# Optimization experiments

Measured on AMD Instinct MI355X. Metric: run time of the kernel, lower is better.

The kernel has to match this reference:

```python
import jax, jax.numpy as jnp
import numpy as np


def _adder2d(x, w, stride, padding):
    """AdderNet 'convolution': out[b,o,i,j] = -sum_p |patch[b,p,i,j] - w[o,p]|.

    x: [B, C, H, W], w: [O, C, kh, kw]. Patches are extracted in (C, kh, kw)
    channel-major order, matching torch.nn.functional.unfold / w.reshape(O, -1).
    """
    O, C, kh, kw = w.shape
    patches = jax.lax.conv_general_dilated_patches(
        x, (kh, kw), (stride, stride), [(padding, padding), (padding, padding)])
    B, P, Ho, Wo = patches.shape  # P = C*kh*kw
    p = patches.reshape(B, P, Ho * Wo)
    wf = w.reshape(O, P)

    def per_out(wo):  # sequential over small O to avoid a [B,O,P,L] blowup
        return -jnp.sum(jnp.abs(p - wo[None, :, None]), axis=1)  # [B, L]

    out = jax.lax.map(per_out, wf)  # [O, B, L]
    return jnp.transpose(out, (1, 0, 2)).reshape(B, O, Ho, Wo)


def setup_inputs() -> dict:
    key = jax.random.key(0)
    ks = jax.random.split(key, 5)
    x = jax.random.normal(ks[0], (4096, 1, 28, 28), dtype=jnp.float32)
    w1 = jax.random.normal(ks[1], (16, 1, 3, 3), dtype=jnp.float32)
    w2 = jax.random.normal(ks[2], (32, 16, 3, 3), dtype=jnp.float32)
    w3 = jax.random.normal(ks[3], (16, 32, 3, 3), dtype=jnp.float32)
    w4 = jax.random.normal(ks[4], (10, 16, 3, 3), dtype=jnp.float32)
    return {"x": x, "w1": w1, "w2": w2, "w3": w3, "w4": w4}


def reference(x, w1, w2, w3, w4):
    h = x - 0.5
    h = jax.nn.relu((_adder2d(h, w1, 2, 0) + 10.0) / 4.0)   # [B,16,13,13]
    h = jax.nn.relu((_adder2d(h, w2, 2, 1) + 130.0) / 8.0)  # [B,32,7,7]
    h = jax.nn.relu((_adder2d(h, w3, 2, 1) + 280.0) / 16.0)  # [B,16,4,4]
    h = _adder2d(h, w4, 2, 0)                                # [B,10,1,1]
    h = h.reshape(h.shape[0], -1)                            # [B,10]
    return jax.nn.log_softmax(h, axis=1)
```

## Files before the change

kernel.cpp:

```cpp
#include <hip/hip_runtime.h>
#include <math.h>


#if defined(__has_builtin)
#if __has_builtin(__builtin_amdgcn_sad_u16)
#define HAS_SAD 1
#endif
#endif

__device__ __forceinline__ unsigned sadu16(unsigned a, unsigned b, unsigned acc) {
#ifdef HAS_SAD
  return __builtin_amdgcn_sad_u16(a, b, acc);
#else
  int al = (int)(a & 0xFFFFu), ah = (int)(a >> 16);
  int bl = (int)(b & 0xFFFFu), bh = (int)(b >> 16);
  return acc + (unsigned)(al > bl ? al - bl : bl - al)
             + (unsigned)(ah > bh ? ah - bh : bh - ah);
#endif
}

__device__ __forceinline__ unsigned quant(float v) {
  return (unsigned)fmaf(v, 1024.0f, 8192.5f);
}
__device__ __forceinline__ unsigned quantx(float v) {
  return (unsigned)fmaf(v, 1024.0f, 7680.5f);
}
__device__ __forceinline__ int imax(int a, int b) { return a > b ? a : b; }
__device__ __forceinline__ int yoff1(int y) { return y * 19 + (y >> 1); }
__device__ __forceinline__ int yoff2(int y) { return y * 9 + (y >> 1); }

#define QPAD 0x20002000u

__global__ void adder_prep(const float* __restrict__ w1, const float* __restrict__ w2,
                           const float* __restrict__ w3, const float* __restrict__ w4,
                           unsigned* __restrict__ qw) {
  int k = blockIdx.x * 256 + threadIdx.x;
  if (k < 96) {
    int o = k / 6, r = k % 6, kh = r >> 1, h = r & 1;
    const float* p = w1 + o * 9 + kh * 3;
    qw[k] = h ? quant(p[2]) : (quant(p[0]) | (quant(p[1]) << 16));
  } else if (k < 2400) {
    int k2 = k - 96, m = k2 / 288, r = k2 % 288, o = r / 9, pk = r % 9;
    int s = o * 144 + 2 * m * 9 + pk;
    qw[k] = quant(w2[s]) | (quant(w2[s + 9]) << 16);
  } else if (k < 4704) {
    int k3 = k - 2400, m2 = k3 / 144, r = k3 % 144, o = r / 9, pk = r % 9;
    int s = o * 288 + 2 * m2 * 9 + pk;
    qw[k] = quant(w3[s]) | (quant(w3[s + 9]) << 16);
  } else if (k < 5424) {
    int k4 = k - 4704, m = k4 / 90, r = k4 % 90, o = r / 9, pk = r % 9;
    int s = o * 144 + 2 * m * 9 + pk;
    qw[k] = quant(w4[s]) | (quant(w4[s + 9]) << 16);
  }
}

__global__ __launch_bounds__(128, 6) void adder_main(
    const float* __restrict__ gx,
    const unsigned* __restrict__ qw,
    float* __restrict__ gout)
{
  __shared__ __align__(16) unsigned sA1[2304];
  __shared__ __align__(16) unsigned sA2[1360];

  const int t = threadIdx.x;
  const int l = t & 63;
  const int wu = __builtin_amdgcn_readfirstlane(t >> 6);
  const int b = blockIdx.x;
  const float* img = gx + (size_t)b * 784;

  for (int k = t; k < 448; k += 128) {
    int plane = k / 56, c = k % 56;
    int y, x;
    if (c < 15)      { y = 0;      x = c; }
    else if (c < 30) { y = 14;     x = c - 15; }
    else if (c < 43) { y = c - 29; x = 0; }
    else             { y = c - 42; x = 14; }
    sA1[plane * 288 + yoff1(y) + x] = QPAD;
  }

  if (l < 52) {
    const int i = l >> 2, jq = l & 3;
    unsigned r[3][5], mw[3][4];
#pragma unroll
    for (int kh = 0; kh < 3; ++kh) {
      const float* rp = img + (2 * i + kh) * 28 + 8 * jq;
      float4 A = *(const float4*)(rp);
      float4 B = *(const float4*)(rp + 4);
      float2 C = *(const float2*)(rp + 8);
      r[kh][0] = quantx(A.x) | (quantx(A.y) << 16);
      r[kh][1] = quantx(A.z) | (quantx(A.w) << 16);
      r[kh][2] = quantx(B.x) | (quantx(B.y) << 16);
      r[kh][3] = quantx(B.z) | (quantx(B.w) << 16);
      r[kh][4] = quantx(C.x) | (quantx(C.y) << 16);
#pragma unroll
      for (int c = 0; c < 4; ++c) mw[kh][c] = r[kh][c + 1] & 0xFFFFu;
    }
    const int dbase = yoff1(i + 1) + 4 * jq + 1;
#pragma unroll 2
    for (int opp = 0; opp < 4; ++opp) {
      const int op = wu * 4 + opp;
      const unsigned* w = qw + op * 12;
      unsigned a0[4], a1[4];
#pragma unroll
      for (int jj = 0; jj < 4; ++jj) { a0[jj] = 0u; a1[jj] = 0u; }
#pragma unroll
      for (int kh = 0; kh < 3; ++kh) {
        unsigned wa01 = w[kh * 2], wa2 = w[kh * 2 + 1];
        unsigned wb01 = w[6 + kh * 2], wb2 = w[6 + kh * 2 + 1];
#pragma unroll
        for (int jj = 0; jj < 4; ++jj) {
          a0[jj] = sadu16(r[kh][jj], wa01, a0[jj]);
          a0[jj] = sadu16(mw[kh][jj], wa2, a0[jj]);
          a1[jj] = sadu16(r[kh][jj], wb01, a1[jj]);
          a1[jj] = sadu16(mw[kh][jj], wb2, a1[jj]);
        }
      }
      unsigned* dst = sA1 + op * 288 + dbase;
#pragma unroll
      for (int jj = 0; jj < 4; ++jj) {
        if (4 * jq + jj < 13) {
          int q0 = imax(10752 - (int)((a0[jj] + 2u) >> 2), 8192);
          int q1 = imax(10752 - (int)((a1[jj] + 2u) >> 2), 8192);
          dst[jj] = (unsigned)q0 | ((unsigned)q1 << 16);
        }
      }
    }
  }
  __syncthreads();

  for (int k = t; k < 512; k += 128) {
    int plane = k >> 5, c = k & 31;
    int y, x;
    if (c < 9)       { y = 0; x = c; }
    else if (c < 18) { y = 8; x = c - 9; }
    else if (c < 25) { y = c - 17; x = 0; }
    else             { y = c - 24; x = 8; }
    sA2[plane * 85 + yoff2(y) + x] = QPAD;
  }

  if (l < 49) {
    const int i = l / 7, j = l % 7;
    unsigned acc[16];
#pragma unroll
    for (int o = 0; o < 16; ++o) acc[o] = 0u;
    const unsigned* qw2 = qw + 96 + wu * 144;
    const unsigned* pb = sA1 + 39 * i + 2 * j;
    const int K1o[3] = {0, 19, 39};
    unsigned p[3][3];
#pragma unroll
    for (int kh = 0; kh < 3; ++kh)
#pragma unroll
      for (int c = 0; c < 3; ++c)
        p[kh][c] = pb[K1o[kh] + c];
#pragma unroll 1
    for (int m = 0; m < 8; ++m) {
      unsigned pn[3][3];
      const unsigned* pbn = pb + (((m + 1) & 7) * 288);
#pragma unroll
      for (int kh = 0; kh < 3; ++kh)
#pragma unroll
        for (int c = 0; c < 3; ++c)
          pn[kh][c] = pbn[K1o[kh] + c];
      const unsigned* wm = qw2 + m * 288;
#pragma unroll
      for (int o = 0; o < 16; ++o) {
        const unsigned* w9 = wm + o * 9;
        unsigned a = acc[o];
#pragma unroll
        for (int kh = 0; kh < 3; ++kh)
#pragma unroll
          for (int c = 0; c < 3; ++c)
            a = sadu16(p[kh][c], w9[kh * 3 + c], a);
        acc[o] = a;
      }
#pragma unroll
      for (int kh = 0; kh < 3; ++kh)
#pragma unroll
        for (int c = 0; c < 3; ++c)
          p[kh][c] = pn[kh][c];
    }
#pragma unroll
    for (int m2 = 0; m2 < 8; ++m2) {
      int q0 = imax(24832 - (int)((acc[2 * m2] + 4u) >> 3), 8192);
      int q1 = imax(24832 - (int)((acc[2 * m2 + 1] + 4u) >> 3), 8192);
      sA2[(wu * 8 + m2) * 85 + yoff2(i + 1) + (j + 1)] = (unsigned)q0 | ((unsigned)q1 << 16);
    }
  }
  __syncthreads();

  {
    const int pos = l & 15, oq = l >> 4;
    const int i = pos >> 2, j = pos & 3;
    const int pr = wu * 4 + oq;
    const unsigned* qw3 = qw + 2400 + pr * 18;
    unsigned acc0 = 0u, acc1 = 0u;
    const unsigned* pb = sA2 + 19 * i + 2 * j;
    const int K2o[3] = {0, 9, 19};
    unsigned p[3][3];
#pragma unroll
    for (int kh = 0; kh < 3; ++kh)
#pragma unroll
      for (int c = 0; c < 3; ++c)
        p[kh][c] = pb[K2o[kh] + c];
#pragma unroll 1
    for (int m2 = 0; m2 < 16; ++m2) {
      unsigned pn[3][3];
      const unsigned* pbn = pb + (((m2 + 1) & 15) * 85);
#pragma unroll
      for (int kh = 0; kh < 3; ++kh)
#pragma unroll
        for (int c = 0; c < 3; ++c)
          pn[kh][c] = pbn[K2o[kh] + c];
      const unsigned* w18 = qw3 + m2 * 144;
#pragma unroll
      for (int kh = 0; kh < 3; ++kh)
#pragma unroll
        for (int c = 0; c < 3; ++c) {
          acc0 = sadu16(p[kh][c], w18[kh * 3 + c], acc0);
          acc1 = sadu16(p[kh][c], w18[9 + kh * 3 + c], acc1);
        }
#pragma unroll
      for (int kh = 0; kh < 3; ++kh)
#pragma unroll
        for (int c = 0; c < 3; ++c)
          p[kh][c] = pn[kh][c];
    }
    int q0 = imax(26112 - (int)((acc0 + 8u) >> 4), 8192);
    int q1 = imax(26112 - (int)((acc1 + 8u) >> 4), 8192);
    sA1[pr * 17 + pos] = (unsigned)q0 | ((unsigned)q1 << 16);
  }
  __syncthreads();

  if (t < 40) {
    const int o = t % 10, mq = t / 10;
    const unsigned* qw4 = qw + 4704;
    unsigned acc = 0u;
#pragma unroll
    for (int mm = 0; mm < 2; ++mm) {
      const int m = mq * 2 + mm;
      const unsigned* a3 = sA1 + m * 17;
      const unsigned* w9 = qw4 + (m * 10 + o) * 9;
#pragma unroll
      for (int kh = 0; kh < 3; ++kh)
#pragma unroll
        for (int kw = 0; kw < 3; ++kw)
          acc = sadu16(a3[kh * 4 + kw], w9[kh * 3 + kw], acc);
    }
    sA1[200 + t] = acc;
  }
  __syncthreads();
  if (t < 10) {
    unsigned s = sA1[200 + t] + sA1[210 + t] + sA1[220 + t] + sA1[230 + t];
    ((float*)sA1)[248 + t] = -(float)s * (1.0f / 1024.0f);
  }
  __syncthreads();
  if (t < 10) {
    const float* lg = (const float*)sA1 + 248;
    float mx = lg[0];
#pragma unroll
    for (int k = 1; k < 10; ++k) mx = fmaxf(mx, lg[k]);
    float sum = 0.0f;
#pragma unroll
    for (int k = 0; k < 10; ++k) sum += __expf(lg[k] - mx);
    gout[(size_t)b * 10 + t] = lg[t] - mx - __logf(sum);
  }
}

extern "C" void kernel_launch(void* const* d_in, const int* in_sizes, int n_in,
                              void* d_out, int out_size, void* d_ws, size_t ws_size,
                              hipStream_t stream) {
  const float* x  = (const float*)d_in[0];
  const float* w1 = (const float*)d_in[1];
  const float* w2 = (const float*)d_in[2];
  const float* w3 = (const float*)d_in[3];
  const float* w4 = (const float*)d_in[4];
  unsigned* qw = (unsigned*)d_ws;
  float* out = (float*)d_out;
  adder_prep<<<22, 256, 0, stream>>>(w1, w2, w3, w4, qw);
  adder_main<<<4096, 128, 0, stream>>>(x, qw, out);
}
```

Before: 110.7 us.

## Pad weight layout for vector loads and use wave shuffles for final softmax

Repacks the layer-2 and layer-3 quantized weights into 12-word padded groups so each output's 9 weights load as three uint4 vector loads. A VGPR zero offset keeps these loads off the scalar path. Layer-1 weights are preloaded into registers and the loop is fully unrolled, the prefetch double-buffering of patch values is dropped, and launch bounds rise to 8 blocks per SIMD. The final reduction and log-softmax now use wave shuffles instead of two extra syncthreads through LDS. Risks include register pressure from the 48-word weight array under the tighter occupancy bound, and more global traffic per vector load.

Result: slower. 161.7 us (+46.0%).

```diff
diff --git a/kernel.cpp b/kernel.cpp
--- a/kernel.cpp
+++ b/kernel.cpp
@@ -39,22 +39,31 @@
     int o = k / 6, r = k % 6, kh = r >> 1, h = r & 1;
     const float* p = w1 + o * 9 + kh * 3;
     qw[k] = h ? quant(p[2]) : (quant(p[0]) | (quant(p[1]) << 16));
-  } else if (k < 2400) {
-    int k2 = k - 96, m = k2 / 288, r = k2 % 288, o = r / 9, pk = r % 9;
-    int s = o * 144 + 2 * m * 9 + pk;
-    qw[k] = quant(w2[s]) | (quant(w2[s + 9]) << 16);
-  } else if (k < 4704) {
-    int k3 = k - 2400, m2 = k3 / 144, r = k3 % 144, o = r / 9, pk = r % 9;
-    int s = o * 288 + 2 * m2 * 9 + pk;
-    qw[k] = quant(w3[s]) | (quant(w3[s + 9]) << 16);
-  } else if (k < 5424) {
-    int k4 = k - 4704, m = k4 / 90, r = k4 % 90, o = r / 9, pk = r % 9;
+  } else if (k < 3168) {
+    int k2 = k - 96, m = k2 / 384, r = k2 % 384, o = r / 12, kk = r % 12;
+    unsigned v = 0u;
+    if (kk < 9) {
+      int s = o * 144 + 2 * m * 9 + kk;
+      v = quant(w2[s]) | (quant(w2[s + 9]) << 16);
+    }
+    qw[k] = v;
+  } else if (k < 6240) {
+    int k3 = k - 3168, m2 = k3 / 192, r = k3 % 192, pr = r / 24, rr = r % 24;
+    int oo = rr / 12, kk = rr % 12;
+    unsigned v = 0u;
+    if (kk < 9) {
+      int s = (2 * pr + oo) * 288 + 2 * m2 * 9 + kk;
+      v = quant(w3[s]) | (quant(w3[s + 9]) << 16);
+    }
+    qw[k] = v;
+  } else if (k < 6960) {
+    int k4 = k - 6240, m = k4 / 90, r = k4 % 90, o = r / 9, pk = r % 9;
     int s = o * 144 + 2 * m * 9 + pk;
     qw[k] = quant(w4[s]) | (quant(w4[s + 9]) << 16);
   }
 }
 
-__global__ __launch_bounds__(128, 6) void adder_main(
+__global__ __launch_bounds__(128, 8) void adder_main(
     const float* __restrict__ gx,
     const unsigned* __restrict__ qw,
     float* __restrict__ gout)
@@ -67,6 +76,9 @@
   const int wu = __builtin_amdgcn_readfirstlane(t >> 6);
   const int b = blockIdx.x;
   const float* img = gx + (size_t)b * 784;
+
+  unsigned voff;
+  asm("v_mov_b32 %0, 0" : "=v"(voff));
 
   for (int k = t; k < 448; k += 128) {
     int plane = k / 56, c = k % 56;
@@ -80,6 +92,10 @@
 
   if (l < 52) {
     const int i = l >> 2, jq = l & 3;
+    unsigned wall[48];
+    const unsigned* wbase = qw + wu * 48;
+#pragma unroll
+    for (int q = 0; q < 48; ++q) wall[q] = wbase[q];
     unsigned r[3][5], mw[3][4];
 #pragma unroll
     for (int kh = 0; kh < 3; ++kh) {
@@ -96,17 +112,16 @@
       for (int c = 0; c < 4; ++c) mw[kh][c] = r[kh][c + 1] & 0xFFFFu;
     }
     const int dbase = yoff1(i + 1) + 4 * jq + 1;
-#pragma unroll 2
+#pragma unroll
     for (int opp = 0; opp < 4; ++opp) {
       const int op = wu * 4 + opp;
-      const unsigned* w = qw + op * 12;
       unsigned a0[4], a1[4];
 #pragma unroll
       for (int jj = 0; jj < 4; ++jj) { a0[jj] = 0u; a1[jj] = 0u; }
 #pragma unroll
       for (int kh = 0; kh < 3; ++kh) {
-        unsigned wa01 = w[kh * 2], wa2 = w[kh * 2 + 1];
-        unsigned wb01 = w[6 + kh * 2], wb2 = w[6 + kh * 2 + 1];
+        unsigned wa01 = wall[opp * 12 + kh * 2], wa2 = wall[opp * 12 + kh * 2 + 1];
+        unsigned wb01 = wall[opp * 12 + 6 + kh * 2], wb2 = wall[opp * 12 + 6 + kh * 2 + 1];
 #pragma unroll
         for (int jj = 0; jj < 4; ++jj) {
           a0[jj] = sadu16(r[kh][jj], wa01, a0[jj]);
@@ -143,41 +158,23 @@
     unsigned acc[16];
 #pragma unroll
     for (int o = 0; o < 16; ++o) acc[o] = 0u;
-    const unsigned* qw2 = qw + 96 + wu * 144;
-    const unsigned* pb = sA1 + 39 * i + 2 * j;
-    const int K1o[3] = {0, 19, 39};
-    unsigned p[3][3];
-#pragma unroll
-    for (int kh = 0; kh < 3; ++kh)
-#pragma unroll
-      for (int c = 0; c < 3; ++c)
-        p[kh][c] = pb[K1o[kh] + c];
+    const unsigned* qw2v = qw + 96 + wu * 192 + voff;
 #pragma unroll 1
     for (int m = 0; m < 8; ++m) {
-      unsigned pn[3][3];
-      const unsigned* pbn = pb + (((m + 1) & 7) * 288);
-#pragma unroll
-      for (int kh = 0; kh < 3; ++kh)
-#pragma unroll
-        for (int c = 0; c < 3; ++c)
-          pn[kh][c] = pbn[K1o[kh] + c];
-      const unsigned* wm = qw2 + m * 288;
+      const unsigned* pb = sA1 + m * 288 + 39 * i + 2 * j;
+      unsigned p00 = pb[0],  p01 = pb[1],  p02 = pb[2];
+      unsigned p10 = pb[19], p11 = pb[20], p12 = pb[21];
+      unsigned p20 = pb[39], p21 = pb[40], p22 = pb[41];
+      const uint4* wm4 = (const uint4*)(qw2v + m * 384);
 #pragma unroll
       for (int o = 0; o < 16; ++o) {
-        const unsigned* w9 = wm + o * 9;
+        uint4 wa = wm4[o * 3], wb = wm4[o * 3 + 1], wc = wm4[o * 3 + 2];
         unsigned a = acc[o];
-#pragma unroll
-        for (int kh = 0; kh < 3; ++kh)
-#pragma unroll
-          for (int c = 0; c < 3; ++c)
-            a = sadu16(p[kh][c], w9[kh * 3 + c], a);
+        a = sadu16(p00, wa.x, a); a = sadu16(p01, wa.y, a); a = sadu16(p02, wa.z, a);
+        a = sadu16(p10, wa.w, a); a = sadu16(p11, wb.x, a); a = sadu16(p12, wb.y, a);
+        a = sadu16(p20, wb.z, a); a = sadu16(p21, wb.w, a); a = sadu16(p22, wc.x, a);
         acc[o] = a;
       }
-#pragma unroll
-      for (int kh = 0; kh < 3; ++kh)
-#pragma unroll
-        for (int c = 0; c < 3; ++c)
-          p[kh][c] = pn[kh][c];
     }
 #pragma unroll
     for (int m2 = 0; m2 < 8; ++m2) {
@@ -192,38 +189,27 @@
     const int pos = l & 15, oq = l >> 4;
     const int i = pos >> 2, j = pos & 3;
     const int pr = wu * 4 + oq;
-    const unsigned* qw3 = qw + 2400 + pr * 18;
+    const unsigned* qw3v = qw + 3168 + pr * 24;
     unsigned acc0 = 0u, acc1 = 0u;
-    const unsigned* pb = sA2 + 19 * i + 2 * j;
-    const int K2o[3] = {0, 9, 19};
-    unsigned p[3][3];
-#pragma unroll
-    for (int kh = 0; kh < 3; ++kh)
-#pragma unroll
-      for (int c = 0; c < 3; ++c)
-        p[kh][c] = pb[K2o[kh] + c];
 #pragma unroll 1
     for (int m2 = 0; m2 < 16; ++m2) {
-      unsigned pn[3][3];
-      const unsigned* pbn = pb + (((m2 + 1) & 15) * 85);
-#pragma unroll
-      for (int kh = 0; kh < 3; ++kh)
-#pragma unroll
-        for (int c = 0; c < 3; ++c)
-          pn[kh][c] = pbn[K2o[kh] + c];
-      const unsigned* w18 = qw3 + m2 * 144;
-#pragma unroll
-      for (int kh = 0; kh < 3; ++kh)
-#pragma unroll
-        for (int c = 0; c < 3; ++c) {
-          acc0 = sadu16(p[kh][c], w18[kh * 3 + c], acc0);
-          acc1 = sadu16(p[kh][c], w18[9 + kh * 3 + c], acc1);
-        }
-#pragma unroll
-      for (int kh = 0; kh < 3; ++kh)
-#pragma unroll
-        for (int c = 0; c < 3; ++c)
-          p[kh][c] = pn[kh][c];
+      const unsigned* pb = sA2 + m2 * 85 + 19 * i + 2 * j;
+      unsigned p00 = pb[0],  p01 = pb[1],  p02 = pb[2];
+      unsigned p10 = pb[9],  p11 = pb[10], p12 = pb[11];
+      unsigned p20 = pb[19], p21 = pb[20], p22 = pb[21];
+      const uint4* w6 = (const uint4*)(qw3v + m2 * 192);
+      uint4 a0 = w6[0], a1 = w6[1], a2 = w6[2];
+      uint4 b0 = w6[3], b1 = w6[4], b2 = w6[5];
+      acc0 = sadu16(p00, a0.x, acc0); acc0 = sadu16(p01, a0.y, acc0);
+      acc0 = sadu16(p02, a0.z, acc0); acc0 = sadu16(p10, a0.w, acc0);
+      acc0 = sadu16(p11, a1.x, acc0); acc0 = sadu16(p12, a1.y, acc0);
+      acc0 = sadu16(p20, a1.z, acc0); acc0 = sadu16(p21, a1.w, acc0);
+      acc0 = sadu16(p22, a2.x, acc0);
+      acc1 = sadu16(p00, b0.x, acc1); acc1 = sadu16(p01, b0.y, acc1);
+      acc1 = sadu16(p02, b0.z, acc1); acc1 = sadu16(p10, b0.w, acc1);
+      acc1 = sadu16(p11, b1.x, acc1); acc1 = sadu16(p12, b1.y, acc1);
+      acc1 = sadu16(p20, b1.z, acc1); acc1 = sadu16(p21, b1.w, acc1);
+      acc1 = sadu16(p22, b2.x, acc1);
     }
     int q0 = imax(26112 - (int)((acc0 + 8u) >> 4), 8192);
     int q1 = imax(26112 - (int)((acc1 + 8u) >> 4), 8192);
@@ -231,38 +217,36 @@
   }
   __syncthreads();
 
-  if (t < 40) {
+  if (wu == 0) {
+    unsigned acc = 0u;
     const int o = t % 10, mq = t / 10;
-    const unsigned* qw4 = qw + 4704;
-    unsigned acc = 0u;
-#pragma unroll
-    for (int mm = 0; mm < 2; ++mm) {
-      const int m = mq * 2 + mm;
-      const unsigned* a3 = sA1 + m * 17;
-      const unsigned* w9 = qw4 + (m * 10 + o) * 9;
-#pragma unroll
-      for (int kh = 0; kh < 3; ++kh)
-#pragma unroll
-        for (int kw = 0; kw < 3; ++kw)
-          acc = sadu16(a3[kh * 4 + kw], w9[kh * 3 + kw], acc);
-    }
-    sA1[200 + t] = acc;
-  }
-  __syncthreads();
-  if (t < 10) {
-    unsigned s = sA1[200 + t] + sA1[210 + t] + sA1[220 + t] + sA1[230 + t];
-    ((float*)sA1)[248 + t] = -(float)s * (1.0f / 1024.0f);
-  }
-  __syncthreads();
-  if (t < 10) {
-    const float* lg = (const float*)sA1 + 248;
-    float mx = lg[0];
-#pragma unroll
-    for (int k = 1; k < 10; ++k) mx = fmaxf(mx, lg[k]);
-    float sum = 0.0f;
-#pragma unroll
-    for (int k = 0; k < 10; ++k) sum += __expf(lg[k] - mx);
-    gout[(size_t)b * 10 + t] = lg[t] - mx - __logf(sum);
+    if (t < 40) {
+      const unsigned* qw4 = qw + 6240;
+#pragma unroll
+      for (int mm = 0; mm < 2; ++mm) {
+        const int m = mq * 2 + mm;
+        const unsigned* a3 = sA1 + m * 17;
+        const unsigned* w9 = qw4 + (m * 10 + o) * 9;
+#pragma unroll
+        for (int kh = 0; kh < 3; ++kh)
+#pragma unroll
+          for (int kw = 0; kw < 3; ++kw)
+            acc = sadu16(a3[kh * 4 + kw], w9[kh * 3 + kw], acc);
+      }
+    }
+    unsigned s = acc + (unsigned)__shfl((int)acc, t + 10)
+                     + (unsigned)__shfl((int)acc, t + 20)
+                     + (unsigned)__shfl((int)acc, t + 30);
+    float lg = (t < 10) ? -(float)s * (1.0f / 1024.0f) : -1e30f;
+    float mx = lg;
+#pragma unroll
+    for (int d = 8; d >= 1; d >>= 1) mx = fmaxf(mx, __shfl_xor(mx, d));
+    float e = (t < 10) ? __expf(lg - mx) : 0.0f;
+    float sum = e;
+#pragma unroll
+    for (int d = 8; d >= 1; d >>= 1) sum += __shfl_xor(sum, d);
+    if (t < 10)
+      gout[(size_t)b * 10 + t] = lg - mx - __logf(sum);
   }
 }
 
@@ -276,6 +260,6 @@
   const float* w4 = (const float*)d_in[4];
   unsigned* qw = (unsigned*)d_ws;
   float* out = (float*)d_out;
-  adder_prep<<<22, 256, 0, stream>>>(w1, w2, w3, w4, qw);
+  adder_prep<<<28, 256, 0, stream>>>(w1, w2, w3, w4, qw);
   adder_main<<<4096, 128, 0, stream>>>(x, qw, out);
 }
```
